# Optimization experiments

Hardware: AMD Instinct MI355X
Metric: run time of the kernel (lower is better)

Reference implementation:

```python
import jax, jax.numpy as jnp
import numpy as np

N, E, G = 50000, 1600000, 64
F_NODE, F_EDGE, ACT = 128, 16, 10
NEG_SLOPE = 0.2  # GATv2Conv default negative_slope
LAYER_DIMS = [(F_NODE, 32), (32, 64), (64, 128)]


def _glorot(k, shape):
    fan_in, fan_out = shape[0], shape[-1]
    s = jnp.sqrt(6.0 / (fan_in + fan_out))
    return jax.random.uniform(k, shape, jnp.float32, -s, s)


def setup_inputs() -> dict:
    key = jax.random.key(0)
    ks = iter(jax.random.split(key, 64))
    inp = {
        "x": jax.random.normal(next(ks), (N, F_NODE), jnp.float32),
        "edge_attr": jax.random.normal(next(ks), (E, F_EDGE), jnp.float32),
        "edge_index": jax.random.randint(next(ks), (2, E), 0, N, jnp.int32),
        "batch": jnp.sort(jax.random.randint(next(ks), (N,), 0, G, jnp.int32)),
    }
    for i, (din, dout) in enumerate(LAYER_DIMS, 1):
        inp[f"Wl{i}"] = _glorot(next(ks), (din, dout))   # lin_l (source transform)
        inp[f"bl{i}"] = jnp.zeros((dout,), jnp.float32)
        inp[f"Wr{i}"] = _glorot(next(ks), (din, dout))   # lin_r (dest transform)
        inp[f"br{i}"] = jnp.zeros((dout,), jnp.float32)
        inp[f"We{i}"] = _glorot(next(ks), (F_EDGE, dout))  # lin_edge (no bias)
        inp[f"att{i}"] = _glorot(next(ks), (1, dout))[0]   # attention vector
        inp[f"bo{i}"] = jnp.zeros((dout,), jnp.float32)    # output bias
    inp["Wv1"] = _glorot(next(ks), (128, 64)); inp["bv1"] = jnp.zeros((64,), jnp.float32)
    inp["Wv2"] = _glorot(next(ks), (64, 1));   inp["bv2"] = jnp.zeros((1,), jnp.float32)
    inp["Wa1"] = _glorot(next(ks), (128, 64)); inp["ba1"] = jnp.zeros((64,), jnp.float32)
    inp["Wa2"] = _glorot(next(ks), (64, ACT)); inp["ba2"] = jnp.zeros((ACT,), jnp.float32)
    return inp


def _gatv2(x, src, dst, ea, Wl, bl, Wr, br, We, att, bo):
    """GATv2Conv, heads=1, concat=True, edge_dim=F_EDGE (eval mode)."""
    xl = x @ Wl + bl                               # [N, D] source-side
    xr = x @ Wr + br                               # [N, D] dest-side
    m = xl[src] + xr[dst] + ea @ We                # [E, D]
    score = (jax.nn.leaky_relu(m, NEG_SLOPE) * att).sum(-1)  # [E]
    # segment softmax over edges grouped by destination node
    mx = jax.lax.stop_gradient(jax.ops.segment_max(score, dst, num_segments=N))
    ex = jnp.exp(score - mx[dst])
    den = jax.ops.segment_sum(ex, dst, num_segments=N)
    alpha = ex / (den[dst] + 1e-16)                # [E]
    out = jax.ops.segment_sum(alpha[:, None] * xl[src], dst, num_segments=N)
    return out + bo


def _forward(x, edge_attr, src, dst, batch, p):
    h = x
    for i in (1, 2, 3):
        h = jax.nn.relu(_gatv2(h, src, dst, edge_attr,
                               p[f"Wl{i}"], p[f"bl{i}"], p[f"Wr{i}"], p[f"br{i}"],
                               p[f"We{i}"], p[f"att{i}"], p[f"bo{i}"]))
    # global mean pool per graph
    cnt = jax.ops.segment_sum(jnp.ones((N,), h.dtype), batch, num_segments=G)
    pooled = jax.ops.segment_sum(h, batch, num_segments=G) / jnp.maximum(cnt, 1.0)[:, None]
    # dueling heads
    v = jax.nn.relu(pooled @ p["Wv1"] + p["bv1"]) @ p["Wv2"] + p["bv2"]      # [G, 1]
    a = jax.nn.relu(pooled @ p["Wa1"] + p["ba1"]) @ p["Wa2"] + p["ba2"]      # [G, ACT]
    return v + (a - a.mean(axis=1, keepdims=True))


def reference(x, edge_attr, edge_index, batch,
              Wl1, bl1, Wr1, br1, We1, att1, bo1,
              Wl2, bl2, Wr2, br2, We2, att2, bo2,
              Wl3, bl3, Wr3, br3, We3, att3, bo3,
              Wv1, bv1, Wv2, bv2, Wa1, ba1, Wa2, ba2):
    p = dict(Wl1=Wl1, bl1=bl1, Wr1=Wr1, br1=br1, We1=We1, att1=att1, bo1=bo1,
             Wl2=Wl2, bl2=bl2, Wr2=Wr2, br2=br2, We2=We2, att2=att2, bo2=bo2,
             Wl3=Wl3, bl3=bl3, Wr3=Wr3, br3=br3, We3=We3, att3=att3, bo3=bo3,
             Wv1=Wv1, bv1=bv1, Wv2=Wv2, bv2=bv2, Wa1=Wa1, ba1=ba1, Wa2=Wa2, ba2=ba2)
    return _forward(x, edge_attr, edge_index[0], edge_index[1], batch, p)
```

## Files before the change

### kernel.cpp

```cpp
#include <hip/hip_runtime.h>
#include <cstdint>
#include <cstddef>

static constexpr int NN = 50000;
static constexpr int NE = 1600000;
static constexpr int NG = 64;
static constexpr int FE = 16;
static constexpr float SLOPE = 0.2f;

template<int DIN, int DOUT>
__global__ __launch_bounds__(256) void k_node_linear(
    const float* __restrict__ h,
    const float* __restrict__ Wl, const float* __restrict__ bl,
    const float* __restrict__ Wr, const float* __restrict__ br,
    float* __restrict__ xl, float* __restrict__ xr)
{
    __shared__ float sW[2 * DIN * DOUT];
    __shared__ float sX[16 * DIN];
    const int n0 = blockIdx.x * 16;

    for (int i = threadIdx.x; i < DIN * DOUT; i += 256) {
        sW[i] = Wl[i];
        sW[DIN * DOUT + i] = Wr[i];
    }
    for (int i = threadIdx.x; i < 16 * DIN; i += 256) {
        int r = i / DIN, k = i % DIN;
        int n = n0 + r;
        sX[i] = (n < NN) ? h[(size_t)n * DIN + k] : 0.0f;
    }
    __syncthreads();

    for (int o = threadIdx.x; o < 16 * DOUT; o += 256) {
        int r = o / DOUT, d = o % DOUT;
        int n = n0 + r;
        if (n >= NN) continue;
        float accl = bl[d], accr = br[d];
        #pragma unroll 8
        for (int k = 0; k < DIN; ++k) {
            float xv = sX[r * DIN + k];
            accl = fmaf(xv, sW[k * DOUT + d], accl);
            accr = fmaf(xv, sW[DIN * DOUT + k * DOUT + d], accr);
        }
        xl[(size_t)n * DOUT + d] = accl;
        xr[(size_t)n * DOUT + d] = accr;
    }
}

__global__ __launch_bounds__(256) void k_count(
    const int* __restrict__ ei, int* __restrict__ cnt)
{
    const int e = blockIdx.x * 256 + threadIdx.x;
    if (e >= NE) return;
    atomicAdd(cnt + ei[NE + e], 1);
}

__global__ __launch_bounds__(1024) void k_scan(
    const int* __restrict__ cnt, int* __restrict__ rowptr)
{
    __shared__ int part[1024];
    const int T = 1024;
    const int C = (NN + T - 1) / T;
    const int t = threadIdx.x;
    const int base = t * C;
    int s = 0;
    for (int i = 0; i < C; ++i) {
        int idx = base + i;
        if (idx < NN) s += cnt[idx];
    }
    part[t] = s;
    __syncthreads();
    for (int off = 1; off < T; off <<= 1) {
        int v = 0;
        if (t >= off) v = part[t - off];
        __syncthreads();
        if (t >= off) part[t] += v;
        __syncthreads();
    }
    int run = (t == 0) ? 0 : part[t - 1];
    for (int i = 0; i < C; ++i) {
        int idx = base + i;
        if (idx < NN) { rowptr[idx] = run; run += cnt[idx]; }
    }
    if (t == T - 1) rowptr[NN] = run;
}

__global__ __launch_bounds__(256) void k_fill(
    const int* __restrict__ ei, const int* __restrict__ rowptr,
    int* __restrict__ woff, int* __restrict__ eids, int* __restrict__ esrc)
{
    const int e = blockIdx.x * 256 + threadIdx.x;
    if (e >= NE) return;
    const int dst = ei[NE + e];
    const int pos = rowptr[dst] + atomicAdd(woff + dst, 1);
    eids[pos] = e;
    esrc[pos] = ei[e];
}

__global__ __launch_bounds__(256) void k_gather_ea(
    const int* __restrict__ eids, const float* __restrict__ ea,
    float* __restrict__ eap)
{
    const long long i = (long long)blockIdx.x * 256 + threadIdx.x;
    if (i >= (long long)NE * 4) return;
    const int p = (int)(i >> 2), q = (int)(i & 3);
    const int e = eids[p];
    *(float4*)(eap + (size_t)p * FE + q * 4) =
        *(const float4*)(ea + (size_t)e * FE + q * 4);
}

template<int D, bool PERM>
__global__ __launch_bounds__(128, 4) void k_gat_fused(
    const int* __restrict__ rowptr, const int* __restrict__ eidx,
    const int* __restrict__ esrc, const float* __restrict__ eaf,
    const float* __restrict__ xl, const float* __restrict__ xr,
    const float* __restrict__ We, const float* __restrict__ att,
    const float* __restrict__ bo, float* __restrict__ hout)
{
    constexpr int SW  = (D >= 128) ? 64 : (D >= 64 ? 32 : 16);
    constexpr int EPW = 64 / SW;
    constexpr int DPL = D / SW;
    constexpr int WPB = 2;
    constexpr int WS  = WPB * EPW;

    __shared__ float sM[WS];
    __shared__ float sL2[WS];
    __shared__ float sAcc[WS][D];

    const int n = blockIdx.x;
    const int t = threadIdx.x;
    const int wave = t >> 6;
    const int lane = t & 63;
    const int sub  = lane / SW;
    const int dl   = lane % SW;
    const int lbase = lane - dl;
    const int stream = wave * EPW + sub;

    float rWe[FE * DPL], rAtt[DPL], rXr[DPL], acc[DPL];
    #pragma unroll
    for (int i = 0; i < DPL; ++i) {
        const int d = dl + SW * i;
        rAtt[i] = att[d];
        rXr[i]  = xr[(size_t)n * D + d];
        acc[i]  = 0.f;
        #pragma unroll
        for (int k = 0; k < FE; ++k) rWe[k * DPL + i] = We[k * D + d];
    }

    const int p0 = rowptr[n], p1 = rowptr[n + 1];
    float m = -3.4e38f, l = 0.f;

    auto load_edge = [&](int p, float (&eav)[FE], float (&rXl)[DPL]) {
        const int s = esrc[p];
        int erow; if constexpr (PERM) erow = p; else erow = eidx[p];
        #pragma unroll
        for (int i = 0; i < DPL; ++i)
            rXl[i] = xl[(size_t)s * D + dl + SW * i];
        if constexpr (SW == 64) {
            const float* ep = eaf + (size_t)(unsigned)__builtin_amdgcn_readfirstlane(erow) * FE;
            #pragma unroll
            for (int k = 0; k < FE; ++k) eav[k] = ep[k];
        } else {
            const float v = eaf[(size_t)erow * FE + (dl & 15)];
            #pragma unroll
            for (int k = 0; k < FE; ++k) eav[k] = __shfl(v, lbase + k, 64);
        }
    };
    auto score_edge = [&](const float (&eav)[FE], const float (&rXl)[DPL]) -> float {
        float sv = 0.f;
        #pragma unroll
        for (int i = 0; i < DPL; ++i) {
            float mm = rXl[i] + rXr[i];
            #pragma unroll
            for (int k = 0; k < FE; ++k) mm = fmaf(eav[k], rWe[k * DPL + i], mm);
            mm = mm > 0.f ? mm : SLOPE * mm;
            sv = fmaf(mm, rAtt[i], sv);
        }
        #pragma unroll
        for (int off = 1; off < SW; off <<= 1) sv += __shfl_xor(sv, off);
        return sv;
    };
    auto sm_update = [&](float sv, const float (&rXl)[DPL]) {
        const float dd = sv - m;
        float wexp;
        if (__builtin_expect(dd > 8.f, 0)) {
            const float r = __expf(-dd);
            #pragma unroll
            for (int i = 0; i < DPL; ++i) acc[i] *= r;
            l *= r; m = sv; wexp = 1.f;
        } else {
            wexp = __expf(dd);
        }
        #pragma unroll
        for (int i = 0; i < DPL; ++i) acc[i] = fmaf(wexp, rXl[i], acc[i]);
        l += wexp;
    };

    int p = p0 + stream;
    for (; p + WS < p1; p += 2 * WS) {
        float eavA[FE], rXlA[DPL], eavB[FE], rXlB[DPL];
        load_edge(p, eavA, rXlA);
        load_edge(p + WS, eavB, rXlB);
        const float svA = score_edge(eavA, rXlA);
        const float svB = score_edge(eavB, rXlB);
        sm_update(svA, rXlA);
        sm_update(svB, rXlB);
    }
    if (p < p1) {
        float eav[FE], rXl[DPL];
        load_edge(p, eav, rXl);
        sm_update(score_edge(eav, rXl), rXl);
    }

    if (dl == 0) sM[stream] = m;
    __syncthreads();
    float mstar = sM[0];
    #pragma unroll
    for (int s2 = 1; s2 < WS; ++s2) mstar = fmaxf(mstar, sM[s2]);
    const float scale = __expf(m - mstar);
    #pragma unroll
    for (int i = 0; i < DPL; ++i) sAcc[stream][dl + SW * i] = acc[i] * scale;
    if (dl == 0) sL2[stream] = l * scale;
    __syncthreads();

    if (t < D) {
        float a = 0.f, lt = 1e-16f;
        #pragma unroll
        for (int s2 = 0; s2 < WS; ++s2) { a += sAcc[s2][t]; lt += sL2[s2]; }
        hout[(size_t)n * D + t] = fmaxf(a / lt + bo[t], 0.f);
    }
}

__global__ __launch_bounds__(128) void k_pool(
    const float* __restrict__ h, const int* __restrict__ batch,
    float* __restrict__ pooled, float* __restrict__ cnt)
{
    constexpr int BLOCKS = 512;
    constexpr int CH = (NN + BLOCKS - 1) / BLOCKS;
    const int t = threadIdx.x;
    const int n0 = blockIdx.x * CH;
    const int n1 = min(NN, n0 + CH);
    if (n0 >= n1) return;

    int g = batch[n0];
    float acc = 0.f, c = 0.f;
    for (int n = n0; n < n1; ++n) {
        const int bg = batch[n];
        if (bg != g) {
            atomicAdd(pooled + g * 128 + t, acc);
            if (t == 0) atomicAdd(cnt + g, c);
            acc = 0.f; c = 0.f; g = bg;
        }
        acc += h[(size_t)n * 128 + t];
        c += 1.f;
    }
    atomicAdd(pooled + g * 128 + t, acc);
    if (t == 0) atomicAdd(cnt + g, c);
}

__global__ __launch_bounds__(128) void k_head(
    const float* __restrict__ pooled, const float* __restrict__ cnt,
    const float* __restrict__ Wv1, const float* __restrict__ bv1,
    const float* __restrict__ Wv2, const float* __restrict__ bv2,
    const float* __restrict__ Wa1, const float* __restrict__ ba1,
    const float* __restrict__ Wa2, const float* __restrict__ ba2,
    float* __restrict__ out)
{
    __shared__ float pr[128];
    __shared__ float hv[64];
    __shared__ float ha[64];
    __shared__ float sA[10];
    __shared__ float sVM[2];
    const int g = blockIdx.x;
    const int t = threadIdx.x;

    const float inv = 1.0f / fmaxf(cnt[g], 1.0f);
    pr[t] = pooled[g * 128 + t] * inv;
    __syncthreads();

    if (t < 64) {
        float sv = bv1[t], sa = ba1[t];
        #pragma unroll 8
        for (int k = 0; k < 128; ++k) {
            float p = pr[k];
            sv = fmaf(p, Wv1[k * 64 + t], sv);
            sa = fmaf(p, Wa1[k * 64 + t], sa);
        }
        hv[t] = fmaxf(sv, 0.0f);
        ha[t] = fmaxf(sa, 0.0f);
    }
    __syncthreads();

    if (t < 10) {
        float av = ba2[t];
        #pragma unroll
        for (int j = 0; j < 64; ++j) av = fmaf(ha[j], Wa2[j * 10 + t], av);
        sA[t] = av;
    }
    if (t == 64) {
        float v = bv2[0];
        #pragma unroll
        for (int j = 0; j < 64; ++j) v = fmaf(hv[j], Wv2[j], v);
        sVM[0] = v;
    }
    __syncthreads();

    if (t == 0) {
        float s = 0.0f;
        #pragma unroll
        for (int j = 0; j < 10; ++j) s += sA[j];
        sVM[1] = s * 0.1f;
    }
    __syncthreads();

    if (t < 10) out[g * 10 + t] = sVM[0] + sA[t] - sVM[1];
}

extern "C" void kernel_launch(void* const* d_in, const int* in_sizes, int n_in,
                              void* d_out, int out_size, void* d_ws, size_t ws_size,
                              hipStream_t stream)
{
    const float* x     = (const float*)d_in[0];
    const float* ea    = (const float*)d_in[1];
    const int*   ei    = (const int*)d_in[2];
    const int*   batch = (const int*)d_in[3];

    float* ws = (float*)d_ws;
    float* xl     = ws;
    float* xr     = xl + (size_t)NN * 128;
    float* hA     = xr + (size_t)NN * 128;
    float* hB     = hA + (size_t)NN * 128;
    float* pooled = hB + (size_t)NN * 64;
    float* cntp   = pooled + (size_t)NG * 128;
    int*   rowptr = (int*)(cntp + NG);
    int*   cnt    = rowptr + (NN + 1);
    int*   woff   = cnt + NN;
    int*   eids   = woff + NN;
    int*   esrc   = eids + NE;
    float* eaperm = (float*)(esrc + NE);

    const size_t need = ((char*)(eaperm + (size_t)NE * FE)) - (char*)d_ws;
    const bool use_perm = (ws_size >= need);

    const int EB = (NE + 255) / 256;

    hipMemsetAsync(cnt, 0, NN * sizeof(int), stream);
    hipMemsetAsync(woff, 0, NN * sizeof(int), stream);
    k_count<<<dim3(EB), dim3(256), 0, stream>>>(ei, cnt);
    k_scan<<<dim3(1), dim3(1024), 0, stream>>>(cnt, rowptr);
    k_fill<<<dim3(EB), dim3(256), 0, stream>>>(ei, rowptr, woff, eids, esrc);
    if (use_perm) {
        const long long tot = (long long)NE * 4;
        k_gather_ea<<<dim3((unsigned)((tot + 255) / 256)), dim3(256), 0, stream>>>(
            eids, ea, eaperm);
    }

#define LAYER(DIN, DOUT, HIN, HOUT, B)                                                   \
    do {                                                                                 \
        k_node_linear<DIN, DOUT><<<dim3((NN + 15) / 16), dim3(256), 0, stream>>>(        \
            HIN, (const float*)d_in[B], (const float*)d_in[(B) + 1],                     \
            (const float*)d_in[(B) + 2], (const float*)d_in[(B) + 3], xl, xr);           \
        if (use_perm)                                                                    \
            k_gat_fused<DOUT, true><<<dim3(NN), dim3(128), 0, stream>>>(                 \
                rowptr, eids, esrc, eaperm, xl, xr, (const float*)d_in[(B) + 4],         \
                (const float*)d_in[(B) + 5], (const float*)d_in[(B) + 6], HOUT);         \
        else                                                                             \
            k_gat_fused<DOUT, false><<<dim3(NN), dim3(128), 0, stream>>>(                \
                rowptr, eids, esrc, ea, xl, xr, (const float*)d_in[(B) + 4],             \
                (const float*)d_in[(B) + 5], (const float*)d_in[(B) + 6], HOUT);         \
    } while (0)

    LAYER(128, 32, x,  hA, 4);
    LAYER(32,  64, hA, hB, 11);
    LAYER(64, 128, hB, hA, 18);

#undef LAYER

    hipMemsetAsync(pooled, 0, NG * 128 * sizeof(float), stream);
    hipMemsetAsync(cntp, 0, NG * sizeof(float), stream);
    k_pool<<<dim3(512), dim3(128), 0, stream>>>(hA, batch, pooled, cntp);
    k_head<<<dim3(NG), dim3(128), 0, stream>>>(
        pooled, cntp,
        (const float*)d_in[25], (const float*)d_in[26],
        (const float*)d_in[27], (const float*)d_in[28],
        (const float*)d_in[29], (const float*)d_in[30],
        (const float*)d_in[31], (const float*)d_in[32],
        (float*)d_out);
}
```

Measured before the change: 1.014 ms.

## Map one wavefront per destination node in GAT kernel with float2 lanes

Restructures the fused GATv2 kernel so each 64-lane wavefront handles one destination node instead of a 128-thread block per node. Each lane owns two output features loaded as float2, and edge attributes are read as float4 rows instead of shuffled. The cross-stream softmax merge uses wave shuffles rather than shared memory and __syncthreads. This aims to cut block count, synchronization and shared-memory traffic, at the cost of fewer concurrent edge streams per node and redundant per-lane edge-attribute loads.

```diff
diff --git a/kernel.cpp b/kernel.cpp
--- a/kernel.cpp
+++ b/kernel.cpp
@@ -116,117 +116,118 @@
     const float* __restrict__ We, const float* __restrict__ att,
     const float* __restrict__ bo, float* __restrict__ hout)
 {
-    constexpr int SW  = (D >= 128) ? 64 : (D >= 64 ? 32 : 16);
+    constexpr int SW  = D / 2;
     constexpr int EPW = 64 / SW;
-    constexpr int DPL = D / SW;
     constexpr int WPB = 2;
-    constexpr int WS  = WPB * EPW;
-
-    __shared__ float sM[WS];
-    __shared__ float sL2[WS];
-    __shared__ float sAcc[WS][D];
-
-    const int n = blockIdx.x;
-    const int t = threadIdx.x;
-    const int wave = t >> 6;
-    const int lane = t & 63;
-    const int sub  = lane / SW;
-    const int dl   = lane % SW;
-    const int lbase = lane - dl;
-    const int stream = wave * EPW + sub;
-
-    float rWe[FE * DPL], rAtt[DPL], rXr[DPL], acc[DPL];
-    #pragma unroll
-    for (int i = 0; i < DPL; ++i) {
-        const int d = dl + SW * i;
-        rAtt[i] = att[d];
-        rXr[i]  = xr[(size_t)n * D + d];
-        acc[i]  = 0.f;
-        #pragma unroll
-        for (int k = 0; k < FE; ++k) rWe[k * DPL + i] = We[k * D + d];
+
+    const int wave = threadIdx.x >> 6;
+    const int lane = threadIdx.x & 63;
+    const int n = blockIdx.x * WPB + wave;
+    if (n >= NN) return;
+    const int sub = lane / SW;
+    const int dl  = lane % SW;
+    const int d0  = 2 * dl;
+
+    float rWe[2 * FE], rAtt[2], rXr[2], acc[2];
+    {
+        const float2 a2 = *(const float2*)(att + d0);
+        rAtt[0] = a2.x; rAtt[1] = a2.y;
+        const float2 x2 = *(const float2*)(xr + (size_t)n * D + d0);
+        rXr[0] = x2.x; rXr[1] = x2.y;
+        #pragma unroll
+        for (int k = 0; k < FE; ++k) {
+            const float2 w2 = *(const float2*)(We + k * D + d0);
+            rWe[2 * k] = w2.x; rWe[2 * k + 1] = w2.y;
+        }
+        acc[0] = acc[1] = 0.f;
     }
 
     const int p0 = rowptr[n], p1 = rowptr[n + 1];
     float m = -3.4e38f, l = 0.f;
 
-    auto load_edge = [&](int p, float (&eav)[FE], float (&rXl)[DPL]) {
+    auto load_edge = [&](int p, float (&eav)[FE], float (&rXl)[2]) {
         const int s = esrc[p];
+        const float2 x2 = *(const float2*)(xl + (size_t)s * D + d0);
+        rXl[0] = x2.x; rXl[1] = x2.y;
         int erow; if constexpr (PERM) erow = p; else erow = eidx[p];
-        #pragma unroll
-        for (int i = 0; i < DPL; ++i)
-            rXl[i] = xl[(size_t)s * D + dl + SW * i];
         if constexpr (SW == 64) {
             const float* ep = eaf + (size_t)(unsigned)__builtin_amdgcn_readfirstlane(erow) * FE;
             #pragma unroll
             for (int k = 0; k < FE; ++k) eav[k] = ep[k];
         } else {
-            const float v = eaf[(size_t)erow * FE + (dl & 15)];
+            const float* ep = eaf + (size_t)erow * FE;
             #pragma unroll
-            for (int k = 0; k < FE; ++k) eav[k] = __shfl(v, lbase + k, 64);
+            for (int k4 = 0; k4 < 4; ++k4) {
+                const float4 v = *(const float4*)(ep + 4 * k4);
+                eav[4 * k4]     = v.x; eav[4 * k4 + 1] = v.y;
+                eav[4 * k4 + 2] = v.z; eav[4 * k4 + 3] = v.w;
+            }
         }
     };
-    auto score_edge = [&](const float (&eav)[FE], const float (&rXl)[DPL]) -> float {
-        float sv = 0.f;
-        #pragma unroll
-        for (int i = 0; i < DPL; ++i) {
-            float mm = rXl[i] + rXr[i];
-            #pragma unroll
-            for (int k = 0; k < FE; ++k) mm = fmaf(eav[k], rWe[k * DPL + i], mm);
-            mm = mm > 0.f ? mm : SLOPE * mm;
-            sv = fmaf(mm, rAtt[i], sv);
-        }
+    auto score_edge = [&](const float (&eav)[FE], const float (&rXl)[2]) -> float {
+        float m0 = rXl[0] + rXr[0], m1 = rXl[1] + rXr[1];
+        #pragma unroll
+        for (int k = 0; k < FE; ++k) {
+            m0 = fmaf(eav[k], rWe[2 * k], m0);
+            m1 = fmaf(eav[k], rWe[2 * k + 1], m1);
+        }
+        m0 = m0 > 0.f ? m0 : SLOPE * m0;
+        m1 = m1 > 0.f ? m1 : SLOPE * m1;
+        float sv = fmaf(m0, rAtt[0], m1 * rAtt[1]);
         #pragma unroll
         for (int off = 1; off < SW; off <<= 1) sv += __shfl_xor(sv, off);
         return sv;
     };
-    auto sm_update = [&](float sv, const float (&rXl)[DPL]) {
+    auto sm_update = [&](float sv, const float (&rXl)[2]) {
         const float dd = sv - m;
         float wexp;
         if (__builtin_expect(dd > 8.f, 0)) {
             const float r = __expf(-dd);
-            #pragma unroll
-            for (int i = 0; i < DPL; ++i) acc[i] *= r;
+            acc[0] *= r; acc[1] *= r;
             l *= r; m = sv; wexp = 1.f;
         } else {
             wexp = __expf(dd);
         }
-        #pragma unroll
-        for (int i = 0; i < DPL; ++i) acc[i] = fmaf(wexp, rXl[i], acc[i]);
+        acc[0] = fmaf(wexp, rXl[0], acc[0]);
+        acc[1] = fmaf(wexp, rXl[1], acc[1]);
         l += wexp;
     };
 
-    int p = p0 + stream;
-    for (; p + WS < p1; p += 2 * WS) {
-        float eavA[FE], rXlA[DPL], eavB[FE], rXlB[DPL];
+    int p = p0 + sub;
+    for (; p + EPW < p1; p += 2 * EPW) {
+        float eavA[FE], rXlA[2], eavB[FE], rXlB[2];
         load_edge(p, eavA, rXlA);
-        load_edge(p + WS, eavB, rXlB);
+        load_edge(p + EPW, eavB, rXlB);
         const float svA = score_edge(eavA, rXlA);
         const float svB = score_edge(eavB, rXlB);
         sm_update(svA, rXlA);
         sm_update(svB, rXlB);
     }
     if (p < p1) {
-        float eav[FE], rXl[DPL];
+        float eav[FE], rXl[2];
         load_edge(p, eav, rXl);
         sm_update(score_edge(eav, rXl), rXl);
     }
 
-    if (dl == 0) sM[stream] = m;
-    __syncthreads();
-    float mstar = sM[0];
     #pragma unroll
-    for (int s2 = 1; s2 < WS; ++s2) mstar = fmaxf(mstar, sM[s2]);
-    const float scale = __expf(m - mstar);
-    #pragma unroll
-    for (int i = 0; i < DPL; ++i) sAcc[stream][dl + SW * i] = acc[i] * scale;
-    if (dl == 0) sL2[stream] = l * scale;
-    __syncthreads();
-
-    if (t < D) {
-        float a = 0.f, lt = 1e-16f;
-        #pragma unroll
-        for (int s2 = 0; s2 < WS; ++s2) { a += sAcc[s2][t]; lt += sL2[s2]; }
-        hout[(size_t)n * D + t] = fmaxf(a / lt + bo[t], 0.f);
+    for (int step = SW; step < 64; step <<= 1) {
+        const float mo = __shfl_xor(m, step);
+        const float mstar = fmaxf(m, mo);
+        const float sc = __expf(m - mstar);
+        acc[0] *= sc; acc[1] *= sc; l *= sc;
+        acc[0] += __shfl_xor(acc[0], step);
+        acc[1] += __shfl_xor(acc[1], step);
+        l += __shfl_xor(l, step);
+        m = mstar;
+    }
+
+    if (lane < SW) {
+        const float inv = 1.0f / (l + 1e-16f);
+        const float2 b2 = *(const float2*)(bo + d0);
+        float2 o;
+        o.x = fmaxf(fmaf(acc[0], inv, b2.x), 0.f);
+        o.y = fmaxf(fmaf(acc[1], inv, b2.y), 0.f);
+        *(float2*)(hout + (size_t)n * D + d0) = o;
     }
 }
 
@@ -354,17 +355,19 @@
             eids, ea, eaperm);
     }
 
+    const int GB = (NN + 1) / 2;
+
 #define LAYER(DIN, DOUT, HIN, HOUT, B)                                                   \
     do {                                                                                 \
         k_node_linear<DIN, DOUT><<<dim3((NN + 15) / 16), dim3(256), 0, stream>>>(        \
             HIN, (const float*)d_in[B], (const float*)d_in[(B) + 1],                     \
             (const float*)d_in[(B) + 2], (const float*)d_in[(B) + 3], xl, xr);           \
         if (use_perm)                                                                    \
-            k_gat_fused<DOUT, true><<<dim3(NN), dim3(128), 0, stream>>>(                 \
+            k_gat_fused<DOUT, true><<<dim3(GB), dim3(128), 0, stream>>>(                 \
                 rowptr, eids, esrc, eaperm, xl, xr, (const float*)d_in[(B) + 4],         \
                 (const float*)d_in[(B) + 5], (const float*)d_in[(B) + 6], HOUT);         \
         else                                                                             \
-            k_gat_fused<DOUT, false><<<dim3(NN), dim3(128), 0, stream>>>(                \
+            k_gat_fused<DOUT, false><<<dim3(GB), dim3(128), 0, stream>>>(                \
                 rowptr, eids, esrc, ea, xl, xr, (const float*)d_in[(B) + 4],             \
                 (const float*)d_in[(B) + 5], (const float*)d_in[(B) + 6], HOUT);         \
     } while (0)
```

Measured after the change: 1.000 ms. About the same (-1.3%).
